# Optimization experiments

Hardware: AMD Instinct MI355X
Metric: run time of the kernel (lower is better)

The kernel has to match this reference:

```python
import jax, jax.numpy as jnp
import numpy as np

B, D, M, NKEYS = 2048, 128, 256, 32768
EST_CONST = np.float32(np.sqrt(np.pi / 2.0) / M)  # sqrt(pi/2)/projection_dim


def setup_inputs() -> dict:
    key = jax.random.key(0)
    k1, k2, k3, k4 = jax.random.split(key, 4)
    query = jax.random.normal(k1, (B, D), dtype=jnp.float32)
    # cached keys are sign-quantized JL sketches (+/-1), as produced by quantize_keys
    cached_keys = jnp.sign(jax.random.normal(k2, (NKEYS, M), dtype=jnp.float32))
    # norms of the original keys: positive, realistic magnitude ~ sqrt(D)
    key_norms = jax.random.uniform(k3, (NKEYS,), dtype=jnp.float32, minval=0.5, maxval=1.5) * np.float32(np.sqrt(D))
    sketch_matrix = jax.random.normal(k4, (M, D), dtype=jnp.float32)
    return {"query": query, "cached_keys": cached_keys, "key_norms": key_norms, "sketch_matrix": sketch_matrix}


def reference(query, cached_keys, key_norms, sketch_matrix):
    # projected_query: [B, M]
    projected_query = jnp.einsum('bd,md->bm', query, sketch_matrix)
    # inner products with quantized keys: [B, NKEYS]
    inner_products = jnp.einsum('bm,nm->bn', projected_query, cached_keys)
    estimated_scores = EST_CONST * key_norms * inner_products  # broadcast over n_keys
    return jax.nn.softmax(estimated_scores, axis=-1)
```

## Files before the change

### kernel.cpp

```cpp
#include <hip/hip_runtime.h>


#define NB 2048
#define DD 128
#define MM 256
#define NK 32768
#define EST_CONST 4.8957583489668673e-03f

typedef _Float16 half8 __attribute__((ext_vector_type(8)));
typedef _Float16 half4v __attribute__((ext_vector_type(4)));
typedef float floatx4 __attribute__((ext_vector_type(4)));

__device__ __forceinline__ void async16(const void* g, void* l) {
    __builtin_amdgcn_global_load_lds(
        (const __attribute__((address_space(1))) unsigned int*)g,
        (__attribute__((address_space(3))) unsigned int*)l,
        16, 0, 0);
}

__global__ void proj_kernel(const float* __restrict__ query,
                            const float* __restrict__ sketch,
                            _Float16* __restrict__ proj) {
    __shared__ float q[DD];
    const int b = blockIdx.x;
    const int t = threadIdx.x;
    if (t < DD) q[t] = query[b * DD + t];
    __syncthreads();
    const float* srow = sketch + t * DD;
    float acc = 0.f;
#pragma unroll
    for (int d = 0; d < DD; d += 4) {
        float4 s4 = *(const float4*)(srow + d);
        acc += s4.x * q[d] + s4.y * q[d + 1] + s4.z * q[d + 2] + s4.w * q[d + 3];
    }
    proj[b * MM + t] = (_Float16)acc;
}

__global__ void cvt_keys(const float* __restrict__ keys, _Float16* __restrict__ kh) {
    const int i = blockIdx.x * 256 + threadIdx.x;
    float4 v = ((const float4*)keys)[i];
    half4v h;
    h.x = (_Float16)v.x; h.y = (_Float16)v.y; h.z = (_Float16)v.z; h.w = (_Float16)v.w;
    ((half4v*)kh)[i] = h;
}

__global__ __launch_bounds__(256, 3)
void stats_kernel(const _Float16* __restrict__ proj,
                  const _Float16* __restrict__ kh,
                  const float* __restrict__ key_norms,
                  float* __restrict__ stats_max,
                  float* __restrict__ stats_sum) {
    __shared__ __align__(16) _Float16 smem[16384];
    __shared__ float red[128][2];
    __shared__ float redS[128][2];
    _Float16* sQ = smem;
    _Float16* sK = smem + 8192;

    const int tid  = threadIdx.x;
    const int lane = tid & 63;
    const int wave = tid >> 6;
    const int quad = lane >> 4;
    const int lc   = lane & 15;
    const int wb   = wave >> 1;
    const int wn   = wave & 1;
    const int cb      = blockIdx.x;
    const int colBase = cb * 128;
    const int rowBase = blockIdx.y * 128;

    floatx4 acc[4][4];
#pragma unroll
    for (int i = 0; i < 4; i++)
#pragma unroll
        for (int j = 0; j < 4; j++) acc[i][j] = (floatx4){0.f, 0.f, 0.f, 0.f};

    const _Float16* gQ[4];
    const _Float16* gK[4];
    int ldsOff[4];
#pragma unroll
    for (int p = 0; p < 4; p++) {
        const int c = p * 256 + tid;
        const int row = c >> 3;
        const int seg = (c & 7) ^ (row & 7);
        gQ[p] = proj + (rowBase + row) * MM + seg * 8;
        gK[p] = kh + (colBase + row) * MM + seg * 8;
        ldsOff[p] = c * 8;
    }

    for (int k0 = 0; k0 < MM; k0 += 64) {
        __syncthreads();
#pragma unroll
        for (int p = 0; p < 4; p++) {
            async16(gQ[p] + k0, &sQ[ldsOff[p]]);
            async16(gK[p] + k0, &sK[ldsOff[p]]);
        }
        __syncthreads();
#pragma unroll
        for (int kk = 0; kk < 2; kk++) {
            const int segSel = ((kk * 4 + quad) ^ (lc & 7)) * 8;
            half8 kf[4], qf[4];
#pragma unroll
            for (int s = 0; s < 4; s++) {
                kf[s] = *(const half8*)&sK[(wn * 64 + s * 16 + lc) * 64 + segSel];
                qf[s] = *(const half8*)&sQ[(wb * 64 + s * 16 + lc) * 64 + segSel];
            }
#pragma unroll
            for (int ib = 0; ib < 4; ib++)
#pragma unroll
                for (int in = 0; in < 4; in++)
                    acc[ib][in] = __builtin_amdgcn_mfma_f32_16x16x32_f16(
                        kf[in], qf[ib], acc[ib][in], 0, 0, 0);
        }
    }

#pragma unroll
    for (int in = 0; in < 4; in++) {
        const float4 nrm = *(const float4*)&key_norms[colBase + wn * 64 + in * 16 + quad * 4];
#pragma unroll
        for (int ib = 0; ib < 4; ib++) {
            acc[ib][in][0] *= EST_CONST * nrm.x;
            acc[ib][in][1] *= EST_CONST * nrm.y;
            acc[ib][in][2] *= EST_CONST * nrm.z;
            acc[ib][in][3] *= EST_CONST * nrm.w;
        }
    }

#pragma unroll
    for (int ib = 0; ib < 4; ib++) {
        float mx = -1e30f;
#pragma unroll
        for (int in = 0; in < 4; in++)
#pragma unroll
            for (int r = 0; r < 4; r++) mx = fmaxf(mx, acc[ib][in][r]);
        mx = fmaxf(mx, __shfl_xor(mx, 16, 64));
        mx = fmaxf(mx, __shfl_xor(mx, 32, 64));
        if (quad == 0) red[wb * 64 + ib * 16 + lc][wn] = mx;
    }
    __syncthreads();
    float mcb[4];
#pragma unroll
    for (int ib = 0; ib < 4; ib++) {
        const int rl = wb * 64 + ib * 16 + lc;
        mcb[ib] = fmaxf(red[rl][0], red[rl][1]);
    }
#pragma unroll
    for (int ib = 0; ib < 4; ib++) {
        float sm = 0.f;
#pragma unroll
        for (int in = 0; in < 4; in++)
#pragma unroll
            for (int r = 0; r < 4; r++) sm += __expf(acc[ib][in][r] - mcb[ib]);
        sm += __shfl_xor(sm, 16, 64);
        sm += __shfl_xor(sm, 32, 64);
        if (quad == 0) redS[wb * 64 + ib * 16 + lc][wn] = sm;
    }
    __syncthreads();
    if (wn == 0 && quad == 0) {
#pragma unroll
        for (int ib = 0; ib < 4; ib++) {
            const int rl = wb * 64 + ib * 16 + lc;
            const int grow = rowBase + rl;
            stats_max[grow * 256 + cb] = mcb[ib];
            stats_sum[grow * 256 + cb] = redS[rl][0] + redS[rl][1];
        }
    }
}

__global__ void combine_stats(const float* __restrict__ smax, const float* __restrict__ ssum,
                              float* __restrict__ rowC) {
    const int lane = threadIdx.x & 63;
    const int row = blockIdx.x * 4 + (threadIdx.x >> 6);
    const float4 mv = ((const float4*)(smax + row * 256))[lane];
    float m = fmaxf(fmaxf(mv.x, mv.y), fmaxf(mv.z, mv.w));
#pragma unroll
    for (int d = 1; d < 64; d <<= 1) m = fmaxf(m, __shfl_xor(m, d, 64));
    const float4 sv = ((const float4*)(ssum + row * 256))[lane];
    float l = sv.x * __expf(mv.x - m) + sv.y * __expf(mv.y - m) +
              sv.z * __expf(mv.z - m) + sv.w * __expf(mv.w - m);
#pragma unroll
    for (int d = 1; d < 64; d <<= 1) l += __shfl_xor(l, d, 64);
    if (lane == 0) rowC[row] = m + __logf(l);
}

__global__ __launch_bounds__(256, 3)
void out_kernel(const _Float16* __restrict__ proj,
                const _Float16* __restrict__ kh,
                const float* __restrict__ key_norms,
                const float* __restrict__ rowC,
                float* __restrict__ out) {
    __shared__ __align__(16) _Float16 smem[16384];
    _Float16* sQ = smem;
    _Float16* sK = smem + 8192;

    const int tid  = threadIdx.x;
    const int lane = tid & 63;
    const int wave = tid >> 6;
    const int quad = lane >> 4;
    const int lc   = lane & 15;
    const int wb   = wave >> 1;
    const int wn   = wave & 1;
    const int cb      = blockIdx.x;
    const int colBase = cb * 128;
    const int rowBase = blockIdx.y * 128;

    floatx4 acc[4][4];
#pragma unroll
    for (int i = 0; i < 4; i++)
#pragma unroll
        for (int j = 0; j < 4; j++) acc[i][j] = (floatx4){0.f, 0.f, 0.f, 0.f};

    const _Float16* gQ[4];
    const _Float16* gK[4];
    int ldsOff[4];
#pragma unroll
    for (int p = 0; p < 4; p++) {
        const int c = p * 256 + tid;
        const int row = c >> 3;
        const int seg = (c & 7) ^ (row & 7);
        gQ[p] = proj + (rowBase + row) * MM + seg * 8;
        gK[p] = kh + (colBase + row) * MM + seg * 8;
        ldsOff[p] = c * 8;
    }

    float cRow[4];
#pragma unroll
    for (int ib = 0; ib < 4; ib++)
        cRow[ib] = rowC[rowBase + wb * 64 + ib * 16 + lc];

    for (int k0 = 0; k0 < MM; k0 += 64) {
        __syncthreads();
#pragma unroll
        for (int p = 0; p < 4; p++) {
            async16(gQ[p] + k0, &sQ[ldsOff[p]]);
            async16(gK[p] + k0, &sK[ldsOff[p]]);
        }
        __syncthreads();
#pragma unroll
        for (int kk = 0; kk < 2; kk++) {
            const int segSel = ((kk * 4 + quad) ^ (lc & 7)) * 8;
            half8 kf[4], qf[4];
#pragma unroll
            for (int s = 0; s < 4; s++) {
                kf[s] = *(const half8*)&sK[(wn * 64 + s * 16 + lc) * 64 + segSel];
                qf[s] = *(const half8*)&sQ[(wb * 64 + s * 16 + lc) * 64 + segSel];
            }
#pragma unroll
            for (int ib = 0; ib < 4; ib++)
#pragma unroll
                for (int in = 0; in < 4; in++)
                    acc[ib][in] = __builtin_amdgcn_mfma_f32_16x16x32_f16(
                        kf[in], qf[ib], acc[ib][in], 0, 0, 0);
        }
    }

#pragma unroll
    for (int in = 0; in < 4; in++) {
        const float4 nrm = *(const float4*)&key_norms[colBase + wn * 64 + in * 16 + quad * 4];
#pragma unroll
        for (int ib = 0; ib < 4; ib++) {
            acc[ib][in][0] *= EST_CONST * nrm.x;
            acc[ib][in][1] *= EST_CONST * nrm.y;
            acc[ib][in][2] *= EST_CONST * nrm.z;
            acc[ib][in][3] *= EST_CONST * nrm.w;
        }
    }

#pragma unroll
    for (int ib = 0; ib < 4; ib++) {
        const int grow = rowBase + wb * 64 + ib * 16 + lc;
        const float c = cRow[ib];
        float* orow = out + (size_t)grow * NK + colBase + wn * 64 + quad * 4;
#pragma unroll
        for (int in = 0; in < 4; in++) {
            floatx4 o;
#pragma unroll
            for (int r = 0; r < 4; r++)
                o[r] = __expf(acc[ib][in][r] - c);
            __builtin_nontemporal_store(o, (floatx4*)(orow + in * 16));
        }
    }
}

extern "C" void kernel_launch(void* const* d_in, const int* in_sizes, int n_in,
                              void* d_out, int out_size, void* d_ws, size_t ws_size,
                              hipStream_t stream) {
    const float* query  = (const float*)d_in[0];
    const float* keys   = (const float*)d_in[1];
    const float* norms  = (const float*)d_in[2];
    const float* sketch = (const float*)d_in[3];
    float* out = (float*)d_out;

    char* ws = (char*)d_ws;
    const size_t MB = 1024 * 1024;
    _Float16* kh   = (_Float16*)(ws);
    _Float16* proj = (_Float16*)(ws + 16 * MB);
    float* smax    = (float*)(ws + 17 * MB);
    float* ssum    = (float*)(ws + 19 * MB);
    float* rowC    = (float*)(ws + 21 * MB);

    hipLaunchKernelGGL(proj_kernel, dim3(NB), dim3(256), 0, stream, query, sketch, proj);
    hipLaunchKernelGGL(cvt_keys, dim3(NK * MM / 4 / 256), dim3(256), 0, stream, keys, kh);
    hipLaunchKernelGGL(stats_kernel, dim3(NK / 128, NB / 128), dim3(256), 0, stream,
                       proj, kh, norms, smax, ssum);
    hipLaunchKernelGGL(combine_stats, dim3(NB / 4), dim3(256), 0, stream,
                       smax, ssum, rowC);
    hipLaunchKernelGGL(out_kernel, dim3(NK / 128, NB / 128), dim3(256), 0, stream,
                       proj, kh, norms, rowC, out);
}
```

Baseline: 409.4 us.

## Double-buffer LDS tiles in stats and output GEMM kernels

Both the stats and output kernels now use two LDS buffers. The global-to-LDS async loads for the next K-slice are issued before the MFMA work on the current slice, so load latency can overlap with compute. This removes one barrier per iteration. In exchange LDS use per block doubles to 64KB, so launch bounds drop to 2 blocks per SM, which lowers occupancy. Correctness depends on the barrier placement ordering async loads against reads of the alternate buffer.

```diff
diff --git a/kernel.cpp b/kernel.cpp
--- a/kernel.cpp
+++ b/kernel.cpp
@@ -10,6 +10,8 @@
 typedef _Float16 half8 __attribute__((ext_vector_type(8)));
 typedef _Float16 half4v __attribute__((ext_vector_type(4)));
 typedef float floatx4 __attribute__((ext_vector_type(4)));
+
+#define BUF_HALVES 16384
 
 __device__ __forceinline__ void async16(const void* g, void* l) {
     __builtin_amdgcn_global_load_lds(
@@ -44,17 +46,16 @@
     ((half4v*)kh)[i] = h;
 }
 
-__global__ __launch_bounds__(256, 3)
+
+__global__ __launch_bounds__(256, 2)
 void stats_kernel(const _Float16* __restrict__ proj,
                   const _Float16* __restrict__ kh,
                   const float* __restrict__ key_norms,
                   float* __restrict__ stats_max,
                   float* __restrict__ stats_sum) {
-    __shared__ __align__(16) _Float16 smem[16384];
+    __shared__ __align__(16) _Float16 smem[2 * BUF_HALVES];
     __shared__ float red[128][2];
     __shared__ float redS[128][2];
-    _Float16* sQ = smem;
-    _Float16* sK = smem + 8192;
 
     const int tid  = threadIdx.x;
     const int lane = tid & 63;
@@ -75,7 +76,7 @@
 
     const _Float16* gQ[4];
     const _Float16* gK[4];
-    int ldsOff[4];
+    int qOff[4];
 #pragma unroll
     for (int p = 0; p < 4; p++) {
         const int c = p * 256 + tid;
@@ -83,17 +84,30 @@
         const int seg = (c & 7) ^ (row & 7);
         gQ[p] = proj + (rowBase + row) * MM + seg * 8;
         gK[p] = kh + (colBase + row) * MM + seg * 8;
-        ldsOff[p] = c * 8;
-    }
-
-    for (int k0 = 0; k0 < MM; k0 += 64) {
-        __syncthreads();
-#pragma unroll
-        for (int p = 0; p < 4; p++) {
-            async16(gQ[p] + k0, &sQ[ldsOff[p]]);
-            async16(gK[p] + k0, &sK[ldsOff[p]]);
-        }
-        __syncthreads();
+        qOff[p] = c * 8;
+    }
+
+#pragma unroll
+    for (int p = 0; p < 4; p++) {
+        async16(gQ[p], &smem[qOff[p]]);
+        async16(gK[p], &smem[8192 + qOff[p]]);
+    }
+    __syncthreads();
+
+    int cur = 0;
+#pragma unroll
+    for (int t = 0; t < 4; ++t) {
+        if (t < 3) {
+            const int k0n = (t + 1) * 64;
+            const int nb = (cur ^ 1) * BUF_HALVES;
+#pragma unroll
+            for (int p = 0; p < 4; p++) {
+                async16(gQ[p] + k0n, &smem[nb + qOff[p]]);
+                async16(gK[p] + k0n, &smem[nb + 8192 + qOff[p]]);
+            }
+        }
+        const _Float16* sQ = smem + cur * BUF_HALVES;
+        const _Float16* sK = sQ + 8192;
 #pragma unroll
         for (int kk = 0; kk < 2; kk++) {
             const int segSel = ((kk * 4 + quad) ^ (lc & 7)) * 8;
@@ -110,6 +124,8 @@
                     acc[ib][in] = __builtin_amdgcn_mfma_f32_16x16x32_f16(
                         kf[in], qf[ib], acc[ib][in], 0, 0, 0);
         }
+        __syncthreads();
+        cur ^= 1;
     }
 
 #pragma unroll
@@ -181,15 +197,13 @@
     if (lane == 0) rowC[row] = m + __logf(l);
 }
 
-__global__ __launch_bounds__(256, 3)
+__global__ __launch_bounds__(256, 2)
 void out_kernel(const _Float16* __restrict__ proj,
                 const _Float16* __restrict__ kh,
                 const float* __restrict__ key_norms,
                 const float* __restrict__ rowC,
                 float* __restrict__ out) {
-    __shared__ __align__(16) _Float16 smem[16384];
-    _Float16* sQ = smem;
-    _Float16* sK = smem + 8192;
+    __shared__ __align__(16) _Float16 smem[2 * BUF_HALVES];
 
     const int tid  = threadIdx.x;
     const int lane = tid & 63;
@@ -210,7 +224,7 @@
 
     const _Float16* gQ[4];
     const _Float16* gK[4];
-    int ldsOff[4];
+    int qOff[4];
 #pragma unroll
     for (int p = 0; p < 4; p++) {
         const int c = p * 256 + tid;
@@ -218,7 +232,7 @@
         const int seg = (c & 7) ^ (row & 7);
         gQ[p] = proj + (rowBase + row) * MM + seg * 8;
         gK[p] = kh + (colBase + row) * MM + seg * 8;
-        ldsOff[p] = c * 8;
+        qOff[p] = c * 8;
     }
 
     float cRow[4];
@@ -226,14 +240,27 @@
     for (int ib = 0; ib < 4; ib++)
         cRow[ib] = rowC[rowBase + wb * 64 + ib * 16 + lc];
 
-    for (int k0 = 0; k0 < MM; k0 += 64) {
-        __syncthreads();
-#pragma unroll
-        for (int p = 0; p < 4; p++) {
-            async16(gQ[p] + k0, &sQ[ldsOff[p]]);
-            async16(gK[p] + k0, &sK[ldsOff[p]]);
-        }
-        __syncthreads();
+#pragma unroll
+    for (int p = 0; p < 4; p++) {
+        async16(gQ[p], &smem[qOff[p]]);
+        async16(gK[p], &smem[8192 + qOff[p]]);
+    }
+    __syncthreads();
+
+    int cur = 0;
+#pragma unroll
+    for (int t = 0; t < 4; ++t) {
+        if (t < 3) {
+            const int k0n = (t + 1) * 64;
+            const int nb = (cur ^ 1) * BUF_HALVES;
+#pragma unroll
+            for (int p = 0; p < 4; p++) {
+                async16(gQ[p] + k0n, &smem[nb + qOff[p]]);
+                async16(gK[p] + k0n, &smem[nb + 8192 + qOff[p]]);
+            }
+        }
+        const _Float16* sQ = smem + cur * BUF_HALVES;
+        const _Float16* sK = sQ + 8192;
 #pragma unroll
         for (int kk = 0; kk < 2; kk++) {
             const int segSel = ((kk * 4 + quad) ^ (lc & 7)) * 8;
@@ -250,6 +277,8 @@
                     acc[ib][in] = __builtin_amdgcn_mfma_f32_16x16x32_f16(
                         kf[in], qf[ib], acc[ib][in], 0, 0, 0);
         }
+        __syncthreads();
+        cur ^= 1;
     }
 
 #pragma unroll
```

Result: slower. 421.2 us (+2.9%).
